# Kernel optimization log

Hardware: AMD Instinct MI355X
Metric: run time of the kernel (lower is better)

## Reference

```python
import jax, jax.numpy as jnp
import numpy as np

N, E, IN, H, C, L = 40000, 640000, 256, 128, 64, 4
ALPHA, LAMB = 0.5, 1.0


def setup_inputs() -> dict:
    key = jax.random.key(0)
    ks = jax.random.split(key, 8)
    x = jax.random.normal(ks[0], (N, IN), jnp.float32)
    src = jax.random.randint(ks[1], (E,), 0, N, jnp.int32)
    dst = jax.random.randint(ks[2], (E,), 0, N, jnp.int32)
    s_in = 1.0 / np.sqrt(IN)
    s_h = 1.0 / np.sqrt(H)
    fc1_w = jax.random.normal(ks[3], (IN, H), jnp.float32) * s_in
    fc1_b = jnp.zeros((H,), jnp.float32)
    W1 = jax.random.normal(ks[4], (L, H, H), jnp.float32) * s_h   # GCN2Conv weight1 per layer
    W2 = jax.random.normal(ks[5], (L, H, H), jnp.float32) * s_h   # GCN2Conv weight2 (initial-residual proj)
    bgc = jnp.zeros((L, H), jnp.float32)                          # GCN2Conv bias per layer
    fc2_w = jax.random.normal(ks[6], (H, C), jnp.float32) * s_h
    fc2_b = jnp.zeros((C,), jnp.float32)
    return dict(x=x, fc1_w=fc1_w, fc1_b=fc1_b, W1=W1, W2=W2, bgc=bgc,
                fc2_w=fc2_w, fc2_b=fc2_b, src=src, dst=dst)


def reference(x, fc1_w, fc1_b, W1, W2, bgc, fc2_w, fc2_b, src, dst):
    ones = jnp.ones((E,), x.dtype)
    # symmetric 'both' normalization: deg_out^{-1/2} on src side, deg_in^{-1/2} on dst side
    deg_out = jnp.clip(jax.ops.segment_sum(ones, src, num_segments=N), 1.0)
    deg_in = jnp.clip(jax.ops.segment_sum(ones, dst, num_segments=N), 1.0)
    norm_s = (deg_out ** -0.5)[:, None]
    norm_d = (deg_in ** -0.5)[:, None]

    # feature_preprocess: dropout (eval = identity) -> fc1 -> relu
    h0 = jax.nn.relu(x @ fc1_w + fc1_b)          # [N, H]
    h = h0
    for l in range(L):
        beta = float(np.log(LAMB / (l + 1) + 1.0))
        identity = h
        # sparse neighbor aggregation (SpMM via gather + segment_sum)
        agg = jax.ops.segment_sum((h * norm_s)[src], dst, num_segments=N) * norm_d
        feat = (1.0 - ALPHA) * agg               # smoothed features
        f0 = ALPHA * h0                          # initial residual
        rst = (1.0 - beta) * (feat + f0) + beta * (feat @ W1[l] + f0 @ W2[l]) + bgc[l]
        h = jax.nn.relu(rst + identity)          # outer residual + activation (dropout eval = identity)
    return h @ fc2_w + fc2_b                     # [N, C]
```

## Files before the change

kernel.cpp:

```cpp
#include <hip/hip_runtime.h>
#include <math.h>

#define N_NODES 40000
#define N_EDGES 640000
#define IN_F 256
#define H_F 128
#define C_F 64
#define L_LAYERS 4
#define SCAN_BLKS 157
#define N_CHUNKS 32
#define CHUNK_E 20000
#define HIST_WORDS 10000

typedef short short8 __attribute__((ext_vector_type(8)));
typedef unsigned short ushort8 __attribute__((ext_vector_type(8)));
typedef float f32x4 __attribute__((ext_vector_type(4)));

__device__ inline short to_bf16(float f) {
    unsigned u = __builtin_bit_cast(unsigned, f);
    unsigned r = (u + 0x7FFFu + ((u >> 16) & 1u)) >> 16;
    return (short)r;
}
__device__ inline float bf16_to_f(unsigned short u) {
    unsigned v = ((unsigned)u) << 16;
    return __builtin_bit_cast(float, v);
}

__device__ inline int block_excl_scan(int v, int* wsum, int* tot) {
    int tid = threadIdx.x;
    int lane = tid & 63, wid = tid >> 6;
    int incl = v;
    #pragma unroll
    for (int off = 1; off < 64; off <<= 1) {
        int t = __shfl_up(incl, off, 64);
        if (lane >= off) incl += t;
    }
    if (lane == 63) wsum[wid] = incl;
    __syncthreads();
    int prefix = 0, total = 0;
    #pragma unroll
    for (int w = 0; w < 4; w++) {
        int s = wsum[w];
        if (w < wid) prefix += s;
        total += s;
    }
    *tot = total;
    return prefix + incl - v;
}

__global__ void prep_w(const float* __restrict__ fc1_w,
                       const float* __restrict__ W1, const float* __restrict__ W2,
                       const float* __restrict__ fc2_w,
                       short* __restrict__ fc1_wT, short* __restrict__ WcatT,
                       short* __restrict__ fc2_wT) {
    int i = blockIdx.x * 256 + threadIdx.x;
    if (i < 128 * 256) {
        int n = i >> 8, k = i & 255;
        fc1_wT[i] = to_bf16(fc1_w[k * H_F + n]);
    }
    if (i < 4 * 128 * 256) {
        int l = i >> 15; int r = i & 32767; int n = r >> 8; int k = r & 255;
        float w = (k < 128) ? W1[l * 16384 + k * H_F + n]
                            : W2[l * 16384 + (k - 128) * H_F + n];
        WcatT[i] = to_bf16(0.5f * w);
    }
    if (i < 64 * 128) {
        int n = i >> 7, k = i & 127;
        fc2_wT[i] = to_bf16(fc2_w[k * C_F + n]);
    }
}

#define CVT8(dstv, p) {                                                         \
    float4 _v0 = *(const float4*)(p); float4 _v1 = *(const float4*)((p) + 4);   \
    dstv[0] = to_bf16(_v0.x); dstv[1] = to_bf16(_v0.y);                         \
    dstv[2] = to_bf16(_v0.z); dstv[3] = to_bf16(_v0.w);                         \
    dstv[4] = to_bf16(_v1.x); dstv[5] = to_bf16(_v1.y);                         \
    dstv[6] = to_bf16(_v1.z); dstv[7] = to_bf16(_v1.w); }

__global__ __launch_bounds__(256) void hist_kernel(const int* __restrict__ src,
                                                   const int* __restrict__ dst,
                                                   int* __restrict__ chunk_dst,
                                                   int* __restrict__ chunk_src,
                                                   unsigned char* __restrict__ lrank8) {
    __shared__ int cntp[HIST_WORDS];
    int blk = blockIdx.x;
    int role_dst = (blk < 32);
    int w = role_dst ? blk : blk - 32;
    const int* idx = role_dst ? dst : src;
    int base = w * CHUNK_E;
    for (int i = threadIdx.x; i < HIST_WORDS; i += 256) cntp[i] = 0;
    __syncthreads();
    if (role_dst) {
        for (int i = threadIdx.x; i < CHUNK_E; i += 256) {
            int d = idx[base + i];
            int sh = (d & 3) * 8;
            int old = atomicAdd(&cntp[d >> 2], 1 << sh);
            lrank8[base + i] = (unsigned char)((old >> sh) & 0xff);
        }
    } else {
        for (int i = threadIdx.x; i < CHUNK_E; i += 256) {
            int s = idx[base + i];
            atomicAdd(&cntp[s >> 2], 1 << ((s & 3) * 8));
        }
    }
    __syncthreads();
    int* outp = role_dst ? (chunk_dst + w * HIST_WORDS) : (chunk_src + w * HIST_WORDS);
    for (int i = threadIdx.x; i < HIST_WORDS; i += 256) outp[i] = cntp[i];
}

__global__ __launch_bounds__(256) void fc1_mfma(const float* __restrict__ x,
                                                const short* __restrict__ wT,
                                                const float* __restrict__ b,
                                                unsigned short* __restrict__ h0b) {
    int tid = threadIdx.x;
    int wave = tid >> 6, lane = tid & 63;
    int rowgrp = wave >> 1, chalf = wave & 1;
    int m = lane & 15, quad = lane >> 4;
    int row = blockIdx.x * 32 + rowgrp * 16 + m;
    const float* xr = x + (size_t)row * IN_F + quad * 8;
    short8 afrag[8];
    #pragma unroll
    for (int ks = 0; ks < 8; ks++) {
        CVT8(afrag[ks], xr + ks * 32);
    }
    #pragma unroll
    for (int ci = 0; ci < 4; ci += 2) {
        int c = chalf * 4 + ci;
        f32x4 acc0 = {0.f, 0.f, 0.f, 0.f};
        f32x4 acc1 = {0.f, 0.f, 0.f, 0.f};
        const short* b0p = wT + (size_t)(c * 16 + m) * IN_F + quad * 8;
        const short* b1p = b0p + 16 * IN_F;
        #pragma unroll
        for (int ks = 0; ks < 8; ks++) {
            short8 b0 = *(const short8*)(b0p + ks * 32);
            short8 b1 = *(const short8*)(b1p + ks * 32);
            acc0 = __builtin_amdgcn_mfma_f32_16x16x32_bf16(afrag[ks], b0, acc0, 0, 0, 0);
            acc1 = __builtin_amdgcn_mfma_f32_16x16x32_bf16(afrag[ks], b1, acc1, 0, 0, 0);
        }
        int col0 = c * 16 + m;
        int rbase = blockIdx.x * 32 + rowgrp * 16 + quad * 4;
        float bg0 = b[col0], bg1 = b[col0 + 16];
        #pragma unroll
        for (int r = 0; r < 4; r++) {
            size_t idx2 = (size_t)(rbase + r) * H_F + col0;
            float v0 = acc0[r] + bg0;
            float v1 = acc1[r] + bg1;
            v0 = v0 > 0.f ? v0 : 0.f;
            v1 = v1 > 0.f ? v1 : 0.f;
            h0b[idx2] = (unsigned short)to_bf16(v0);
            h0b[idx2 + 16] = (unsigned short)to_bf16(v1);
        }
    }
}

__global__ __launch_bounds__(256) void scan1(const int* __restrict__ chunk_dst,
                                             const int* __restrict__ chunk_src,
                                             unsigned short* __restrict__ base16,
                                             float* __restrict__ rsq_in,
                                             float* __restrict__ rsq_out,
                                             int* __restrict__ row_local,
                                             int* __restrict__ blk_sum) {
    __shared__ int wsum[4];
    int n = blockIdx.x * 256 + threadIdx.x;
    int deg_in = 0;
    if (n < N_NODES) {
        int word = n >> 2, sh = (n & 3) * 8;
        int run = 0;
        #pragma unroll 4
        for (int w = 0; w < N_CHUNKS; w++) {
            int v = (chunk_dst[w * HIST_WORDS + word] >> sh) & 0xff;
            base16[w * N_NODES + n] = (unsigned short)run;
            run += v;
        }
        deg_in = run;
        int so = 0;
        #pragma unroll 4
        for (int w = 0; w < N_CHUNKS; w++)
            so += (chunk_src[w * HIST_WORDS + word] >> sh) & 0xff;
        rsq_in[n] = 1.0f / sqrtf((float)(deg_in < 1 ? 1 : deg_in));
        rsq_out[n] = 1.0f / sqrtf((float)(so < 1 ? 1 : so));
    }
    int tot;
    int excl = block_excl_scan(deg_in, wsum, &tot);
    if (n < N_NODES) row_local[n] = excl;
    if (threadIdx.x == 0) blk_sum[blockIdx.x] = tot;
}

__global__ __launch_bounds__(256) void fill_fused(const int* __restrict__ src,
                                                  const int* __restrict__ dst,
                                                  const unsigned char* __restrict__ lrank8,
                                                  const unsigned short* __restrict__ base16,
                                                  const int* __restrict__ row_local,
                                                  const int* __restrict__ blk_sum,
                                                  const float* __restrict__ rsq_in,
                                                  const float* __restrict__ rsq_out,
                                                  int* __restrict__ col,
                                                  float* __restrict__ wv,
                                                  int* __restrict__ row_ptr) {
    __shared__ int wsum[4];
    __shared__ int blk_offL[SCAN_BLKS];
    int tid = threadIdx.x;
    int v = (tid < SCAN_BLKS) ? blk_sum[tid] : 0;
    int tot;
    int excl = block_excl_scan(v, wsum, &tot);
    if (tid < SCAN_BLKS) blk_offL[tid] = excl;
    __syncthreads();

    int blk = blockIdx.x;
    if (blk < 2500) {
        int e = blk * 256 + tid;
        int w = e / CHUNK_E;
        int s = src[e], d = dst[e];
        int rp = blk_offL[d >> 8] + row_local[d] + (int)base16[w * N_NODES + d]
               + (int)lrank8[e];
        col[rp] = s;
        wv[rp] = rsq_out[s] * rsq_in[d];
        return;
    }
    int n = (blk - 2500) * 256 + tid;
    if (n < N_NODES) row_ptr[n] = blk_offL[n >> 8] + row_local[n];
    if (blk == 2500 && tid == 0) row_ptr[N_NODES] = N_EDGES;
}

__global__ __launch_bounds__(256) void spmm_kernel(const unsigned short* __restrict__ hb,
                                                   const int* __restrict__ row_ptr,
                                                   const int* __restrict__ col,
                                                   const float* __restrict__ wv,
                                                   unsigned short* __restrict__ aggb) {
    int wave = threadIdx.x >> 6, lane = threadIdx.x & 63;
    int slot = lane >> 4, fi = lane & 15;
    int n = blockIdx.x * 4 + wave;
    int e0 = row_ptr[n], e1 = row_ptr[n + 1];
    float a[8] = {};
    for (int e = e0 + slot; e < e1; e += 16) {
        int eb = e + 4, ec = e + 8, ed = e + 12;
        int c0 = col[e];                    float w0 = wv[e];
        int c1 = (eb < e1) ? col[eb] : c0;  float w1 = (eb < e1) ? wv[eb] : 0.f;
        int c2 = (ec < e1) ? col[ec] : c0;  float w2 = (ec < e1) ? wv[ec] : 0.f;
        int c3 = (ed < e1) ? col[ed] : c0;  float w3 = (ed < e1) ? wv[ed] : 0.f;
        ushort8 u0 = *(const ushort8*)(hb + (size_t)c0 * H_F + fi * 8);
        ushort8 u1 = *(const ushort8*)(hb + (size_t)c1 * H_F + fi * 8);
        ushort8 u2 = *(const ushort8*)(hb + (size_t)c2 * H_F + fi * 8);
        ushort8 u3 = *(const ushort8*)(hb + (size_t)c3 * H_F + fi * 8);
        #pragma unroll
        for (int j = 0; j < 8; j++) {
            a[j] += w0 * bf16_to_f(u0[j]) + w1 * bf16_to_f(u1[j])
                  + w2 * bf16_to_f(u2[j]) + w3 * bf16_to_f(u3[j]);
        }
    }
    #pragma unroll
    for (int mask = 16; mask <= 32; mask <<= 1) {
        #pragma unroll
        for (int j = 0; j < 8; j++) a[j] += __shfl_xor(a[j], mask, 64);
    }
    if (slot == 0) {
        ushort8 r;
        #pragma unroll
        for (int j = 0; j < 8; j++) r[j] = (unsigned short)to_bf16(a[j]);
        *(ushort8*)(aggb + (size_t)n * H_F + fi * 8) = r;
    }
}

__global__ __launch_bounds__(256) void combine_mfma(const unsigned short* __restrict__ aggb,
                                                    const unsigned short* __restrict__ h0b,
                                                    const unsigned short* __restrict__ hb,
                                                    const short* __restrict__ wT,
                                                    const float* __restrict__ bgc,
                                                    float beta,
                                                    unsigned short* __restrict__ h_outb) {
    int tid = threadIdx.x;
    int wave = tid >> 6, lane = tid & 63;
    int rowgrp = wave >> 1, chalf = wave & 1;
    int m = lane & 15, quad = lane >> 4;
    int row = blockIdx.x * 32 + rowgrp * 16 + m;
    const unsigned short* aggr = aggb + (size_t)row * H_F + quad * 8;
    const unsigned short* h0r  = h0b + (size_t)row * H_F + quad * 8;
    short8 afrag[8];
    #pragma unroll
    for (int ks = 0; ks < 4; ks++) {
        afrag[ks] = __builtin_bit_cast(short8, *(const ushort8*)(aggr + ks * 32));
        afrag[ks + 4] = __builtin_bit_cast(short8, *(const ushort8*)(h0r + ks * 32));
    }
    float omb = 1.f - beta;
    #pragma unroll
    for (int ci = 0; ci < 4; ci += 2) {
        int c = chalf * 4 + ci;
        f32x4 acc0 = {0.f, 0.f, 0.f, 0.f};
        f32x4 acc1 = {0.f, 0.f, 0.f, 0.f};
        const short* b0p = wT + (size_t)(c * 16 + m) * 256 + quad * 8;
        const short* b1p = b0p + 16 * 256;
        #pragma unroll
        for (int ks = 0; ks < 8; ks++) {
            short8 b0 = *(const short8*)(b0p + ks * 32);
            short8 b1 = *(const short8*)(b1p + ks * 32);
            acc0 = __builtin_amdgcn_mfma_f32_16x16x32_bf16(afrag[ks], b0, acc0, 0, 0, 0);
            acc1 = __builtin_amdgcn_mfma_f32_16x16x32_bf16(afrag[ks], b1, acc1, 0, 0, 0);
        }
        int col0 = c * 16 + m;
        int rbase = blockIdx.x * 32 + rowgrp * 16 + quad * 4;
        float bg0 = bgc[col0], bg1 = bgc[col0 + 16];
        #pragma unroll
        for (int r = 0; r < 4; r++) {
            size_t idx = (size_t)(rbase + r) * H_F + col0;
            float s0 = 0.5f * (bf16_to_f(aggb[idx]) + bf16_to_f(h0b[idx]));
            float s1 = 0.5f * (bf16_to_f(aggb[idx + 16]) + bf16_to_f(h0b[idx + 16]));
            float v0 = omb * s0 + beta * acc0[r] + bg0 + bf16_to_f(hb[idx]);
            float v1 = omb * s1 + beta * acc1[r] + bg1 + bf16_to_f(hb[idx + 16]);
            v0 = v0 > 0.f ? v0 : 0.f;
            v1 = v1 > 0.f ? v1 : 0.f;
            h_outb[idx] = (unsigned short)to_bf16(v0);
            h_outb[idx + 16] = (unsigned short)to_bf16(v1);
        }
    }
}

__global__ __launch_bounds__(256) void fc2_mfma(const unsigned short* __restrict__ hb,
                                                const short* __restrict__ wT,
                                                const float* __restrict__ b,
                                                float* __restrict__ out) {
    int tid = threadIdx.x;
    int wave = tid >> 6, lane = tid & 63;
    int m = lane & 15, quad = lane >> 4;
    int row = blockIdx.x * 64 + wave * 16 + m;
    const unsigned short* hr = hb + (size_t)row * H_F + quad * 8;
    short8 afrag[4];
    #pragma unroll
    for (int ks = 0; ks < 4; ks++) {
        afrag[ks] = __builtin_bit_cast(short8, *(const ushort8*)(hr + ks * 32));
    }
    #pragma unroll
    for (int c = 0; c < 4; c += 2) {
        f32x4 acc0 = {0.f, 0.f, 0.f, 0.f};
        f32x4 acc1 = {0.f, 0.f, 0.f, 0.f};
        const short* b0p = wT + (size_t)(c * 16 + m) * H_F + quad * 8;
        const short* b1p = b0p + 16 * H_F;
        #pragma unroll
        for (int ks = 0; ks < 4; ks++) {
            short8 b0 = *(const short8*)(b0p + ks * 32);
            short8 b1 = *(const short8*)(b1p + ks * 32);
            acc0 = __builtin_amdgcn_mfma_f32_16x16x32_bf16(afrag[ks], b0, acc0, 0, 0, 0);
            acc1 = __builtin_amdgcn_mfma_f32_16x16x32_bf16(afrag[ks], b1, acc1, 0, 0, 0);
        }
        int col0 = c * 16 + m;
        int rbase = blockIdx.x * 64 + wave * 16 + quad * 4;
        float bg0 = b[col0], bg1 = b[col0 + 16];
        #pragma unroll
        for (int r = 0; r < 4; r++) {
            size_t idx = (size_t)(rbase + r) * C_F + col0;
            out[idx] = acc0[r] + bg0;
            out[idx + 16] = acc1[r] + bg1;
        }
    }
}

extern "C" void kernel_launch(void* const* d_in, const int* in_sizes, int n_in,
                              void* d_out, int out_size, void* d_ws, size_t ws_size,
                              hipStream_t stream) {
    const float* x     = (const float*)d_in[0];
    const float* fc1_w = (const float*)d_in[1];
    const float* fc1_b = (const float*)d_in[2];
    const float* W1    = (const float*)d_in[3];
    const float* W2    = (const float*)d_in[4];
    const float* bgc   = (const float*)d_in[5];
    const float* fc2_w = (const float*)d_in[6];
    const float* fc2_b = (const float*)d_in[7];
    const int*   src   = (const int*)d_in[8];
    const int*   dst   = (const int*)d_in[9];
    float* out = (float*)d_out;

    char* p = (char*)d_ws;
    auto alloc = [&](size_t bytes) {
        char* r = p;
        p += (bytes + 255) & ~(size_t)255;
        return r;
    };
    int*   chunk_dst = (int*)alloc((size_t)N_CHUNKS * HIST_WORDS * 4);
    int*   chunk_src = (int*)alloc((size_t)N_CHUNKS * HIST_WORDS * 4);
    unsigned short* base16 = (unsigned short*)alloc((size_t)N_CHUNKS * N_NODES * 2);
    unsigned char*  lrank8 = (unsigned char*)alloc((size_t)N_EDGES);
    float* rsq_in  = (float*)alloc((size_t)N_NODES * 4);
    float* rsq_out = (float*)alloc((size_t)N_NODES * 4);
    int*   row_ptr   = (int*)alloc((size_t)(N_NODES + 1) * 4);
    int*   row_local = (int*)alloc((size_t)N_NODES * 4);
    int*   blk_sum   = (int*)alloc((size_t)SCAN_BLKS * 4);
    int*   col     = (int*)alloc((size_t)N_EDGES * 4);
    float* wv      = (float*)alloc((size_t)N_EDGES * 4);
    unsigned short* aggb = (unsigned short*)alloc((size_t)N_NODES * H_F * 2);
    unsigned short* h0b  = (unsigned short*)alloc((size_t)N_NODES * H_F * 2);
    unsigned short* hAb  = (unsigned short*)alloc((size_t)N_NODES * H_F * 2);
    unsigned short* hBb  = (unsigned short*)alloc((size_t)N_NODES * H_F * 2);
    short* fc1_wT  = (short*)alloc((size_t)128 * 256 * 2);
    short* WcatT   = (short*)alloc((size_t)4 * 128 * 256 * 2);
    short* fc2_wT  = (short*)alloc((size_t)64 * 128 * 2);

    prep_w<<<512, 256, 0, stream>>>(fc1_w, W1, W2, fc2_w, fc1_wT, WcatT, fc2_wT);
    hist_kernel<<<64, 256, 0, stream>>>(src, dst, chunk_dst, chunk_src, lrank8);
    fc1_mfma<<<N_NODES / 32, 256, 0, stream>>>(x, fc1_wT, fc1_b, h0b);
    scan1<<<SCAN_BLKS, 256, 0, stream>>>(chunk_dst, chunk_src, base16,
                                         rsq_in, rsq_out, row_local, blk_sum);
    fill_fused<<<2500 + SCAN_BLKS, 256, 0, stream>>>(src, dst, lrank8, base16,
                                                     row_local, blk_sum, rsq_in, rsq_out,
                                                     col, wv, row_ptr);

    const unsigned short* sp_in[4] = {h0b, hAb, hBb, hAb};
    unsigned short* out_b[4]       = {hAb, hBb, hAb, hBb};
    for (int l = 0; l < L_LAYERS; l++) {
        float beta = (float)log(1.0 / (double)(l + 1) + 1.0);
        spmm_kernel<<<N_NODES / 4, 256, 0, stream>>>(sp_in[l], row_ptr, col, wv, aggb);
        combine_mfma<<<N_NODES / 32, 256, 0, stream>>>(aggb, h0b, sp_in[l],
                                                       WcatT + (size_t)l * 128 * 256,
                                                       bgc + (size_t)l * H_F,
                                                       beta, out_b[l]);
    }
    fc2_mfma<<<N_NODES / 64, 256, 0, stream>>>(hBb, fc2_wT, fc2_b, out);
}
```

Before: 383.3 us.

## Store pre-scaled features, 16-bit column indices, and fuse setup kernels

Hidden states are now stored pre-multiplied by deg_out^-1/2, so the SpMM no longer reads per-edge weights. Column indices shrink to 16-bit and the float weight array is removed, which cuts per-edge gather traffic. Setup kernels are merged: weight prep with the histogram, fc1 with the scan, and h0 pre-scaling into the fill kernel. The histogram chunk count doubles and the scan now writes 32-bit bases. Folding beta into the weights and adding an extra bf16 rounding of the scaled states changes numerics slightly, and the per-layer state passes through an additional scale and unscale.

Result: faster. 370.7 us (-3.3%).

```diff
diff --git a/kernel.cpp b/kernel.cpp
--- a/kernel.cpp
+++ b/kernel.cpp
@@ -8,8 +8,8 @@
 #define C_F 64
 #define L_LAYERS 4
 #define SCAN_BLKS 157
-#define N_CHUNKS 32
-#define CHUNK_E 20000
+#define N_CHUNKS 64
+#define CHUNK_E 10000
 #define HIST_WORDS 10000
 
 typedef short short8 __attribute__((ext_vector_type(8)));
@@ -46,28 +46,6 @@
     }
     *tot = total;
     return prefix + incl - v;
-}
-
-__global__ void prep_w(const float* __restrict__ fc1_w,
-                       const float* __restrict__ W1, const float* __restrict__ W2,
-                       const float* __restrict__ fc2_w,
-                       short* __restrict__ fc1_wT, short* __restrict__ WcatT,
-                       short* __restrict__ fc2_wT) {
-    int i = blockIdx.x * 256 + threadIdx.x;
-    if (i < 128 * 256) {
-        int n = i >> 8, k = i & 255;
-        fc1_wT[i] = to_bf16(fc1_w[k * H_F + n]);
-    }
-    if (i < 4 * 128 * 256) {
-        int l = i >> 15; int r = i & 32767; int n = r >> 8; int k = r & 255;
-        float w = (k < 128) ? W1[l * 16384 + k * H_F + n]
-                            : W2[l * 16384 + (k - 128) * H_F + n];
-        WcatT[i] = to_bf16(0.5f * w);
-    }
-    if (i < 64 * 128) {
-        int n = i >> 7, k = i & 127;
-        fc2_wT[i] = to_bf16(fc2_w[k * C_F + n]);
-    }
 }
 
 #define CVT8(dstv, p) {                                                         \
@@ -77,46 +55,117 @@
     dstv[4] = to_bf16(_v1.x); dstv[5] = to_bf16(_v1.y);                         \
     dstv[6] = to_bf16(_v1.z); dstv[7] = to_bf16(_v1.w); }
 
-__global__ __launch_bounds__(256) void hist_kernel(const int* __restrict__ src,
-                                                   const int* __restrict__ dst,
-                                                   int* __restrict__ chunk_dst,
-                                                   int* __restrict__ chunk_src,
-                                                   unsigned char* __restrict__ lrank8) {
+__global__ __launch_bounds__(256) void prep_hist(const int* __restrict__ src,
+                                                 const int* __restrict__ dst,
+                                                 int* __restrict__ chunk_dst,
+                                                 int* __restrict__ chunk_src,
+                                                 unsigned char* __restrict__ lrank8,
+                                                 const float* __restrict__ fc1_w,
+                                                 const float* __restrict__ W1,
+                                                 const float* __restrict__ W2,
+                                                 const float* __restrict__ fc2_w,
+                                                 float s0, float s1, float s2, float s3,
+                                                 short* __restrict__ fc1_wT,
+                                                 short* __restrict__ WcatT,
+                                                 short* __restrict__ fc2_wT) {
     __shared__ int cntp[HIST_WORDS];
     int blk = blockIdx.x;
-    int role_dst = (blk < 32);
-    int w = role_dst ? blk : blk - 32;
-    const int* idx = role_dst ? dst : src;
-    int base = w * CHUNK_E;
-    for (int i = threadIdx.x; i < HIST_WORDS; i += 256) cntp[i] = 0;
-    __syncthreads();
-    if (role_dst) {
-        for (int i = threadIdx.x; i < CHUNK_E; i += 256) {
-            int d = idx[base + i];
-            int sh = (d & 3) * 8;
-            int old = atomicAdd(&cntp[d >> 2], 1 << sh);
-            lrank8[base + i] = (unsigned char)((old >> sh) & 0xff);
-        }
-    } else {
-        for (int i = threadIdx.x; i < CHUNK_E; i += 256) {
-            int s = idx[base + i];
-            atomicAdd(&cntp[s >> 2], 1 << ((s & 3) * 8));
-        }
-    }
-    __syncthreads();
-    int* outp = role_dst ? (chunk_dst + w * HIST_WORDS) : (chunk_src + w * HIST_WORDS);
-    for (int i = threadIdx.x; i < HIST_WORDS; i += 256) outp[i] = cntp[i];
-}
-
-__global__ __launch_bounds__(256) void fc1_mfma(const float* __restrict__ x,
+    if (blk < 128) {
+        int role_dst = (blk < 64);
+        int w = role_dst ? blk : blk - 64;
+        const int* idx = role_dst ? dst : src;
+        int base = w * CHUNK_E;
+        for (int i = threadIdx.x; i < HIST_WORDS; i += 256) cntp[i] = 0;
+        __syncthreads();
+        if (role_dst) {
+            for (int i = threadIdx.x; i < CHUNK_E; i += 256) {
+                int d = idx[base + i];
+                int sh = (d & 3) * 8;
+                int old = atomicAdd(&cntp[d >> 2], 1 << sh);
+                lrank8[base + i] = (unsigned char)((old >> sh) & 0xff);
+            }
+        } else {
+            for (int i = threadIdx.x; i < CHUNK_E; i += 256) {
+                int s = idx[base + i];
+                atomicAdd(&cntp[s >> 2], 1 << ((s & 3) * 8));
+            }
+        }
+        __syncthreads();
+        int* outp = role_dst ? (chunk_dst + w * HIST_WORDS) : (chunk_src + w * HIST_WORDS);
+        for (int i = threadIdx.x; i < HIST_WORDS; i += 256) outp[i] = cntp[i];
+        return;
+    }
+    int i = (blk - 128) * 256 + threadIdx.x;
+    if (i < 128 * 256) {
+        int n = i >> 8, k = i & 255;
+        fc1_wT[i] = to_bf16(fc1_w[k * H_F + n]);
+    }
+    if (i < 4 * 128 * 256) {
+        int l = i >> 15; int r = i & 32767; int n = r >> 8; int k = r & 255;
+        float sc = (l == 0) ? s0 : (l == 1) ? s1 : (l == 2) ? s2 : s3;
+        float w = (k < 128) ? W1[l * 16384 + k * H_F + n]
+                            : W2[l * 16384 + (k - 128) * H_F + n];
+        WcatT[i] = to_bf16(sc * w);
+    }
+    if (i < 64 * 128) {
+        int n = i >> 7, k = i & 127;
+        fc2_wT[i] = to_bf16(fc2_w[k * C_F + n]);
+    }
+}
+
+__global__ __launch_bounds__(256) void fc1_scan(const float* __restrict__ x,
                                                 const short* __restrict__ wT,
                                                 const float* __restrict__ b,
-                                                unsigned short* __restrict__ h0b) {
+                                                unsigned short* __restrict__ h0b,
+                                                const int* __restrict__ chunk_dst,
+                                                const int* __restrict__ chunk_src,
+                                                int* __restrict__ base32,
+                                                float* __restrict__ rsq_in,
+                                                float* __restrict__ rsq_out,
+                                                float* __restrict__ sq_out,
+                                                int* __restrict__ row_local,
+                                                int* __restrict__ blk_sum) {
+    __shared__ int wsum[4];
+    int blk = blockIdx.x;
+    if (blk >= 1250) {
+        int sb = blk - 1250;
+        int n = sb * 256 + threadIdx.x;
+        int deg = 0, word = 0, sh = 0;
+        if (n < N_NODES) {
+            word = n >> 2; sh = (n & 3) * 8;
+            #pragma unroll 4
+            for (int w = 0; w < N_CHUNKS; w++)
+                deg += (chunk_dst[w * HIST_WORDS + word] >> sh) & 0xff;
+        }
+        int tot;
+        int excl = block_excl_scan(deg, wsum, &tot);
+        if (n < N_NODES) {
+            row_local[n] = excl;
+            int run = excl;
+            #pragma unroll 4
+            for (int w = 0; w < N_CHUNKS; w++) {
+                int v = (chunk_dst[w * HIST_WORDS + word] >> sh) & 0xff;
+                base32[(size_t)w * N_NODES + n] = run;
+                run += v;
+            }
+            int so = 0;
+            #pragma unroll 4
+            for (int w = 0; w < N_CHUNKS; w++)
+                so += (chunk_src[w * HIST_WORDS + word] >> sh) & 0xff;
+            float fd = (float)(deg < 1 ? 1 : deg);
+            float fs = (float)(so < 1 ? 1 : so);
+            rsq_in[n] = 1.0f / sqrtf(fd);
+            rsq_out[n] = 1.0f / sqrtf(fs);
+            sq_out[n] = sqrtf(fs);
+        }
+        if (threadIdx.x == 0) blk_sum[sb] = tot;
+        return;
+    }
     int tid = threadIdx.x;
     int wave = tid >> 6, lane = tid & 63;
     int rowgrp = wave >> 1, chalf = wave & 1;
     int m = lane & 15, quad = lane >> 4;
-    int row = blockIdx.x * 32 + rowgrp * 16 + m;
+    int row = blk * 32 + rowgrp * 16 + m;
     const float* xr = x + (size_t)row * IN_F + quad * 8;
     short8 afrag[8];
     #pragma unroll
@@ -138,7 +187,7 @@
             acc1 = __builtin_amdgcn_mfma_f32_16x16x32_bf16(afrag[ks], b1, acc1, 0, 0, 0);
         }
         int col0 = c * 16 + m;
-        int rbase = blockIdx.x * 32 + rowgrp * 16 + quad * 4;
+        int rbase = blk * 32 + rowgrp * 16 + quad * 4;
         float bg0 = b[col0], bg1 = b[col0 + 16];
         #pragma unroll
         for (int r = 0; r < 4; r++) {
@@ -153,57 +202,26 @@
     }
 }
 
-__global__ __launch_bounds__(256) void scan1(const int* __restrict__ chunk_dst,
-                                             const int* __restrict__ chunk_src,
-                                             unsigned short* __restrict__ base16,
-                                             float* __restrict__ rsq_in,
-                                             float* __restrict__ rsq_out,
-                                             int* __restrict__ row_local,
-                                             int* __restrict__ blk_sum) {
-    __shared__ int wsum[4];
-    int n = blockIdx.x * 256 + threadIdx.x;
-    int deg_in = 0;
-    if (n < N_NODES) {
-        int word = n >> 2, sh = (n & 3) * 8;
-        int run = 0;
-        #pragma unroll 4
-        for (int w = 0; w < N_CHUNKS; w++) {
-            int v = (chunk_dst[w * HIST_WORDS + word] >> sh) & 0xff;
-            base16[w * N_NODES + n] = (unsigned short)run;
-            run += v;
-        }
-        deg_in = run;
-        int so = 0;
-        #pragma unroll 4
-        for (int w = 0; w < N_CHUNKS; w++)
-            so += (chunk_src[w * HIST_WORDS + word] >> sh) & 0xff;
-        rsq_in[n] = 1.0f / sqrtf((float)(deg_in < 1 ? 1 : deg_in));
-        rsq_out[n] = 1.0f / sqrtf((float)(so < 1 ? 1 : so));
-    }
-    int tot;
-    int excl = block_excl_scan(deg_in, wsum, &tot);
-    if (n < N_NODES) row_local[n] = excl;
-    if (threadIdx.x == 0) blk_sum[blockIdx.x] = tot;
-}
-
 __global__ __launch_bounds__(256) void fill_fused(const int* __restrict__ src,
                                                   const int* __restrict__ dst,
                                                   const unsigned char* __restrict__ lrank8,
-                                                  const unsigned short* __restrict__ base16,
+                                                  const int* __restrict__ base32,
                                                   const int* __restrict__ row_local,
                                                   const int* __restrict__ blk_sum,
-                                                  const float* __restrict__ rsq_in,
+                                                  unsigned short* __restrict__ col16,
+                                                  int* __restrict__ row_ptr,
+                                                  const unsigned short* __restrict__ h0b,
                                                   const float* __restrict__ rsq_out,
-                                                  int* __restrict__ col,
-                                                  float* __restrict__ wv,
-                                                  int* __restrict__ row_ptr) {
+                                                  unsigned short* __restrict__ h0s) {
     __shared__ int wsum[4];
     __shared__ int blk_offL[SCAN_BLKS];
     int tid = threadIdx.x;
-    int v = (tid < SCAN_BLKS) ? blk_sum[tid] : 0;
-    int tot;
-    int excl = block_excl_scan(v, wsum, &tot);
-    if (tid < SCAN_BLKS) blk_offL[tid] = excl;
+    {
+        int v = (tid < SCAN_BLKS) ? blk_sum[tid] : 0;
+        int tot;
+        int excl = block_excl_scan(v, wsum, &tot);
+        if (tid < SCAN_BLKS) blk_offL[tid] = excl;
+    }
     __syncthreads();
 
     int blk = blockIdx.x;
@@ -211,21 +229,29 @@
         int e = blk * 256 + tid;
         int w = e / CHUNK_E;
         int s = src[e], d = dst[e];
-        int rp = blk_offL[d >> 8] + row_local[d] + (int)base16[w * N_NODES + d]
-               + (int)lrank8[e];
-        col[rp] = s;
-        wv[rp] = rsq_out[s] * rsq_in[d];
+        int rp = blk_offL[d >> 8] + base32[(size_t)w * N_NODES + d] + (int)lrank8[e];
+        col16[rp] = (unsigned short)s;
         return;
     }
-    int n = (blk - 2500) * 256 + tid;
-    if (n < N_NODES) row_ptr[n] = blk_offL[n >> 8] + row_local[n];
-    if (blk == 2500 && tid == 0) row_ptr[N_NODES] = N_EDGES;
-}
-
-__global__ __launch_bounds__(256) void spmm_kernel(const unsigned short* __restrict__ hb,
+    if (blk < 2657) {
+        int n = (blk - 2500) * 256 + tid;
+        if (n < N_NODES) row_ptr[n] = blk_offL[n >> 8] + row_local[n];
+        if (blk == 2500 && tid == 0) row_ptr[N_NODES] = N_EDGES;
+        return;
+    }
+    int j = (blk - 2657) * 2048 + tid * 8;
+    ushort8 u = *(const ushort8*)(h0b + j);
+    float rs = rsq_out[j >> 7];
+    ushort8 o;
+    #pragma unroll
+    for (int jj = 0; jj < 8; jj++) o[jj] = (unsigned short)to_bf16(rs * bf16_to_f(u[jj]));
+    *(ushort8*)(h0s + j) = o;
+}
+
+__global__ __launch_bounds__(256) void spmm_kernel(const unsigned short* __restrict__ hs,
                                                    const int* __restrict__ row_ptr,
-                                                   const int* __restrict__ col,
-                                                   const float* __restrict__ wv,
+                                                   const unsigned short* __restrict__ col16,
+                                                   const float* __restrict__ rsq_in,
                                                    unsigned short* __restrict__ aggb) {
     int wave = threadIdx.x >> 6, lane = threadIdx.x & 63;
     int slot = lane >> 4, fi = lane & 15;
@@ -234,17 +260,17 @@
     float a[8] = {};
     for (int e = e0 + slot; e < e1; e += 16) {
         int eb = e + 4, ec = e + 8, ed = e + 12;
-        int c0 = col[e];                    float w0 = wv[e];
-        int c1 = (eb < e1) ? col[eb] : c0;  float w1 = (eb < e1) ? wv[eb] : 0.f;
-        int c2 = (ec < e1) ? col[ec] : c0;  float w2 = (ec < e1) ? wv[ec] : 0.f;
-        int c3 = (ed < e1) ? col[ed] : c0;  float w3 = (ed < e1) ? wv[ed] : 0.f;
-        ushort8 u0 = *(const ushort8*)(hb + (size_t)c0 * H_F + fi * 8);
-        ushort8 u1 = *(const ushort8*)(hb + (size_t)c1 * H_F + fi * 8);
-        ushort8 u2 = *(const ushort8*)(hb + (size_t)c2 * H_F + fi * 8);
-        ushort8 u3 = *(const ushort8*)(hb + (size_t)c3 * H_F + fi * 8);
+        int c0 = col16[e];
+        int c1 = (eb < e1) ? col16[eb] : c0;  float w1 = (eb < e1) ? 1.f : 0.f;
+        int c2 = (ec < e1) ? col16[ec] : c0;  float w2 = (ec < e1) ? 1.f : 0.f;
+        int c3 = (ed < e1) ? col16[ed] : c0;  float w3 = (ed < e1) ? 1.f : 0.f;
+        ushort8 u0 = *(const ushort8*)(hs + (size_t)c0 * H_F + fi * 8);
+        ushort8 u1 = *(const ushort8*)(hs + (size_t)c1 * H_F + fi * 8);
+        ushort8 u2 = *(const ushort8*)(hs + (size_t)c2 * H_F + fi * 8);
+        ushort8 u3 = *(const ushort8*)(hs + (size_t)c3 * H_F + fi * 8);
         #pragma unroll
         for (int j = 0; j < 8; j++) {
-            a[j] += w0 * bf16_to_f(u0[j]) + w1 * bf16_to_f(u1[j])
+            a[j] += bf16_to_f(u0[j]) + w1 * bf16_to_f(u1[j])
                   + w2 * bf16_to_f(u2[j]) + w3 * bf16_to_f(u3[j]);
         }
     }
@@ -254,20 +280,23 @@
         for (int j = 0; j < 8; j++) a[j] += __shfl_xor(a[j], mask, 64);
     }
     if (slot == 0) {
+        float rs = rsq_in[n];
         ushort8 r;
         #pragma unroll
-        for (int j = 0; j < 8; j++) r[j] = (unsigned short)to_bf16(a[j]);
+        for (int j = 0; j < 8; j++) r[j] = (unsigned short)to_bf16(rs * a[j]);
         *(ushort8*)(aggb + (size_t)n * H_F + fi * 8) = r;
     }
 }
 
 __global__ __launch_bounds__(256) void combine_mfma(const unsigned short* __restrict__ aggb,
                                                     const unsigned short* __restrict__ h0b,
-                                                    const unsigned short* __restrict__ hb,
+                                                    const unsigned short* __restrict__ hs_in,
                                                     const short* __restrict__ wT,
                                                     const float* __restrict__ bgc,
-                                                    float beta,
-                                                    unsigned short* __restrict__ h_outb) {
+                                                    const float* __restrict__ rsq_out,
+                                                    const float* __restrict__ sq_out,
+                                                    float omb5,
+                                                    unsigned short* __restrict__ hs_out) {
     int tid = threadIdx.x;
     int wave = tid >> 6, lane = tid & 63;
     int rowgrp = wave >> 1, chalf = wave & 1;
@@ -281,7 +310,6 @@
         afrag[ks] = __builtin_bit_cast(short8, *(const ushort8*)(aggr + ks * 32));
         afrag[ks + 4] = __builtin_bit_cast(short8, *(const ushort8*)(h0r + ks * 32));
     }
-    float omb = 1.f - beta;
     #pragma unroll
     for (int ci = 0; ci < 4; ci += 2) {
         int c = chalf * 4 + ci;
@@ -301,20 +329,24 @@
         float bg0 = bgc[col0], bg1 = bgc[col0 + 16];
         #pragma unroll
         for (int r = 0; r < 4; r++) {
-            size_t idx = (size_t)(rbase + r) * H_F + col0;
-            float s0 = 0.5f * (bf16_to_f(aggb[idx]) + bf16_to_f(h0b[idx]));
-            float s1 = 0.5f * (bf16_to_f(aggb[idx + 16]) + bf16_to_f(h0b[idx + 16]));
-            float v0 = omb * s0 + beta * acc0[r] + bg0 + bf16_to_f(hb[idx]);
-            float v1 = omb * s1 + beta * acc1[r] + bg1 + bf16_to_f(hb[idx + 16]);
+            int rw = rbase + r;
+            size_t idx = (size_t)rw * H_F + col0;
+            float sq = sq_out[rw];
+            float rsq = rsq_out[rw];
+            float s0 = bf16_to_f(aggb[idx]) + bf16_to_f(h0b[idx]);
+            float s1 = bf16_to_f(aggb[idx + 16]) + bf16_to_f(h0b[idx + 16]);
+            float v0 = omb5 * s0 + acc0[r] + bg0 + sq * bf16_to_f(hs_in[idx]);
+            float v1 = omb5 * s1 + acc1[r] + bg1 + sq * bf16_to_f(hs_in[idx + 16]);
             v0 = v0 > 0.f ? v0 : 0.f;
             v1 = v1 > 0.f ? v1 : 0.f;
-            h_outb[idx] = (unsigned short)to_bf16(v0);
-            h_outb[idx + 16] = (unsigned short)to_bf16(v1);
-        }
-    }
-}
-
-__global__ __launch_bounds__(256) void fc2_mfma(const unsigned short* __restrict__ hb,
+            hs_out[idx] = (unsigned short)to_bf16(rsq * v0);
+            hs_out[idx + 16] = (unsigned short)to_bf16(rsq * v1);
+        }
+    }
+}
+
+__global__ __launch_bounds__(256) void fc2_mfma(const unsigned short* __restrict__ hs,
+                                                const float* __restrict__ sq_out,
                                                 const short* __restrict__ wT,
                                                 const float* __restrict__ b,
                                                 float* __restrict__ out) {
@@ -322,11 +354,14 @@
     int wave = tid >> 6, lane = tid & 63;
     int m = lane & 15, quad = lane >> 4;
     int row = blockIdx.x * 64 + wave * 16 + m;
-    const unsigned short* hr = hb + (size_t)row * H_F + quad * 8;
+    const unsigned short* hr = hs + (size_t)row * H_F + quad * 8;
+    float sq = sq_out[row];
     short8 afrag[4];
     #pragma unroll
     for (int ks = 0; ks < 4; ks++) {
-        afrag[ks] = __builtin_bit_cast(short8, *(const ushort8*)(hr + ks * 32));
+        ushort8 u = *(const ushort8*)(hr + ks * 32);
+        #pragma unroll
+        for (int j = 0; j < 8; j++) afrag[ks][j] = to_bf16(sq * bf16_to_f(u[j]));
     }
     #pragma unroll
     for (int c = 0; c < 4; c += 2) {
@@ -376,41 +411,51 @@
     };
     int*   chunk_dst = (int*)alloc((size_t)N_CHUNKS * HIST_WORDS * 4);
     int*   chunk_src = (int*)alloc((size_t)N_CHUNKS * HIST_WORDS * 4);
-    unsigned short* base16 = (unsigned short*)alloc((size_t)N_CHUNKS * N_NODES * 2);
-    unsigned char*  lrank8 = (unsigned char*)alloc((size_t)N_EDGES);
+    int*   base32    = (int*)alloc((size_t)N_CHUNKS * N_NODES * 4);
+    unsigned char* lrank8 = (unsigned char*)alloc((size_t)N_EDGES);
     float* rsq_in  = (float*)alloc((size_t)N_NODES * 4);
     float* rsq_out = (float*)alloc((size_t)N_NODES * 4);
+    float* sq_out  = (float*)alloc((size_t)N_NODES * 4);
     int*   row_ptr   = (int*)alloc((size_t)(N_NODES + 1) * 4);
     int*   row_local = (int*)alloc((size_t)N_NODES * 4);
     int*   blk_sum   = (int*)alloc((size_t)SCAN_BLKS * 4);
-    int*   col     = (int*)alloc((size_t)N_EDGES * 4);
-    float* wv      = (float*)alloc((size_t)N_EDGES * 4);
+    unsigned short* col16 = (unsigned short*)alloc((size_t)N_EDGES * 2);
     unsigned short* aggb = (unsigned short*)alloc((size_t)N_NODES * H_F * 2);
     unsigned short* h0b  = (unsigned short*)alloc((size_t)N_NODES * H_F * 2);
-    unsigned short* hAb  = (unsigned short*)alloc((size_t)N_NODES * H_F * 2);
-    unsigned short* hBb  = (unsigned short*)alloc((size_t)N_NODES * H_F * 2);
+    unsigned short* h0s  = (unsigned short*)alloc((size_t)N_NODES * H_F * 2);
+    unsigned short* hAs  = (unsigned short*)alloc((size_t)N_NODES * H_F * 2);
+    unsigned short* hBs  = (unsigned short*)alloc((size_t)N_NODES * H_F * 2);
     short* fc1_wT  = (short*)alloc((size_t)128 * 256 * 2);
     short* WcatT   = (short*)alloc((size_t)4 * 128 * 256 * 2);
     short* fc2_wT  = (short*)alloc((size_t)64 * 128 * 2);
 
-    prep_w<<<512, 256, 0, stream>>>(fc1_w, W1, W2, fc2_w, fc1_wT, WcatT, fc2_wT);
-    hist_kernel<<<64, 256, 0, stream>>>(src, dst, chunk_dst, chunk_src, lrank8);
-    fc1_mfma<<<N_NODES / 32, 256, 0, stream>>>(x, fc1_wT, fc1_b, h0b);
-    scan1<<<SCAN_BLKS, 256, 0, stream>>>(chunk_dst, chunk_src, base16,
-                                         rsq_in, rsq_out, row_local, blk_sum);
-    fill_fused<<<2500 + SCAN_BLKS, 256, 0, stream>>>(src, dst, lrank8, base16,
-                                                     row_local, blk_sum, rsq_in, rsq_out,
-                                                     col, wv, row_ptr);
-
-    const unsigned short* sp_in[4] = {h0b, hAb, hBb, hAb};
-    unsigned short* out_b[4]       = {hAb, hBb, hAb, hBb};
+    float beta[4], wscale[4], omb5[4];
+    for (int l = 0; l < 4; l++) {
+        beta[l] = (float)log(1.0 / (double)(l + 1) + 1.0);
+        wscale[l] = 0.5f * beta[l];
+        omb5[l] = 0.5f * (1.f - beta[l]);
+    }
+
+    prep_hist<<<640, 256, 0, stream>>>(src, dst, chunk_dst, chunk_src, lrank8,
+                                       fc1_w, W1, W2, fc2_w,
+                                       wscale[0], wscale[1], wscale[2], wscale[3],
+                                       fc1_wT, WcatT, fc2_wT);
+    fc1_scan<<<1407, 256, 0, stream>>>(x, fc1_wT, fc1_b, h0b,
+                                       chunk_dst, chunk_src, base32,
+                                       rsq_in, rsq_out, sq_out, row_local, blk_sum);
+    fill_fused<<<5157, 256, 0, stream>>>(src, dst, lrank8, base32, row_local, blk_sum,
+                                         col16, row_ptr, h0b, rsq_out, h0s);
+
+    const unsigned short* sp_in[4] = {h0s, hAs, hBs, hAs};
+    unsigned short* out_b[4]       = {hAs, hBs, hAs, hBs};
     for (int l = 0; l < L_LAYERS; l++) {
-        float beta = (float)log(1.0 / (double)(l + 1) + 1.0);
-        spmm_kernel<<<N_NODES / 4, 256, 0, stream>>>(sp_in[l], row_ptr, col, wv, aggb);
+        spmm_kernel<<<N_NODES / 4, 256, 0, stream>>>(sp_in[l], row_ptr, col16,
+                                                     rsq_in, aggb);
         combine_mfma<<<N_NODES / 32, 256, 0, stream>>>(aggb, h0b, sp_in[l],
                                                        WcatT + (size_t)l * 128 * 256,
                                                        bgc + (size_t)l * H_F,
-                                                       beta, out_b[l]);
-    }
-    fc2_mfma<<<N_NODES / 64, 256, 0, stream>>>(hBb, fc2_wT, fc2_b, out);
-}
+                                                       rsq_out, sq_out, omb5[l],
+                                                       out_b[l]);
+    }
+    fc2_mfma<<<N_NODES / 64, 256, 0, stream>>>(hBs, sq_out, fc2_wT, fc2_b, out);
+}
```
